# Performance work log

Hardware: AMD Instinct MI355X
Metric: run time of the kernel (lower is better)

The kernel has to match this reference:

```python
import jax, jax.numpy as jnp
import numpy as np


def setup_inputs() -> dict:
    key = jax.random.key(0)
    k1, k2 = jax.random.split(key)
    x1 = jax.random.normal(k1, (8192, 256), dtype=jnp.float32)
    x2 = jax.random.normal(k2, (8192, 256), dtype=jnp.float32)
    return {"x1": x1, "x2": x2}


def reference(x1, x2):
    # Euclidean distance matrix, equivalent to torch.cdist(x1, x2, p=2.0).
    # GEMM-based expansion: ||a-b||^2 = ||a||^2 + ||b||^2 - 2 a.b
    sq1 = jnp.sum(x1 * x1, axis=-1, keepdims=True)          # [N, 1]
    sq2 = jnp.sum(x2 * x2, axis=-1, keepdims=True)          # [M, 1]
    cross = jnp.einsum('nd,md->nm', x1, x2)                 # [N, M]
    d2 = sq1 + sq2.T - 2.0 * cross
    d2 = jnp.maximum(d2, 0.0)  # guard tiny negatives from cancellation
    return jnp.sqrt(d2)
```

## Files before the change

### kernel.cpp

```cpp
#include <hip/hip_runtime.h>


typedef __bf16 v8bf __attribute__((ext_vector_type(8)));
typedef float v4f __attribute__((ext_vector_type(4)));

#define NROWS 8192
#define KDIM  256
#define TILE  128
#define BK    64

typedef const __attribute__((address_space(1))) ushort* gas_ushort_p;
typedef __attribute__((address_space(3))) ushort* las_ushort_p;

__device__ __forceinline__ void async_load16(const ushort* g, ushort* l) {
    __builtin_amdgcn_global_load_lds((gas_ushort_p)g, (las_ushort_p)l, 16, 0, 0);
}

__device__ __forceinline__ ushort f2bf_rne(float f) {
    union { float f; unsigned u; } a; a.f = f;
    unsigned u = a.u + 0x7fffu + ((a.u >> 16) & 1u);
    return (ushort)(u >> 16);
}

__global__ __launch_bounds__(256) void cvt_norm_kernel(
    const float* __restrict__ x, ushort* __restrict__ xb, float* __restrict__ sq) {
    const int wave = threadIdx.x >> 6;
    const int lane = threadIdx.x & 63;
    const int row  = blockIdx.x * 4 + wave;
    const float4 v = ((const float4*)(x + (size_t)row * KDIM))[lane];
    float s = v.x * v.x + v.y * v.y + v.z * v.z + v.w * v.w;
#pragma unroll
    for (int off = 32; off; off >>= 1) s += __shfl_down(s, off);
    if (lane == 0) sq[row] = s;
    ushort4 o;
    o.x = f2bf_rne(v.x); o.y = f2bf_rne(v.y);
    o.z = f2bf_rne(v.z); o.w = f2bf_rne(v.w);
    ((ushort4*)(xb + (size_t)row * KDIM))[lane] = o;
}

__global__ __launch_bounds__(256) void cdist_mfma_kernel(
    const ushort* __restrict__ A,
    const ushort* __restrict__ B,
    const float* __restrict__ sq1,
    const float* __restrict__ sq2,
    float* __restrict__ out) {
    __shared__ ushort As[TILE * BK];
    __shared__ ushort Bs[TILE * BK];

    const int bm = blockIdx.x, bn = blockIdx.y;
    const int tid  = threadIdx.x;
    const int wave = tid >> 6;
    const int lane = tid & 63;
    const int wr = wave >> 1;
    const int wc = wave & 1;

    const int lrow = lane >> 3;
    const int lk   = (lane & 7) * 8;

    v4f acc[4][4];
#pragma unroll
    for (int i = 0; i < 4; ++i)
#pragma unroll
        for (int j = 0; j < 4; ++j) acc[i][j] = (v4f){0.f, 0.f, 0.f, 0.f};

    const int half = lane >> 4;
    const int mrow = lane & 15;

    for (int kt = 0; kt < KDIM; kt += BK) {
        __syncthreads();
#pragma unroll
        for (int c = 0; c < 4; ++c) {
            const int rbase = wave * 32 + c * 8;
            const ushort* ga =
                A + (size_t)(bm * TILE + rbase + lrow) * KDIM + kt + lk;
            const ushort* gb =
                B + (size_t)(bn * TILE + rbase + lrow) * KDIM + kt + lk;
            async_load16(ga, &As[rbase * BK]);
            async_load16(gb, &Bs[rbase * BK]);
        }
        __syncthreads();
#pragma unroll
        for (int kk = 0; kk < BK; kk += 32) {
            v8bf a[4], b[4];
#pragma unroll
            for (int i = 0; i < 4; ++i) {
                a[i] = *(const v8bf*)&As[(wr * 64 + i * 16 + mrow) * BK + kk + half * 8];
                b[i] = *(const v8bf*)&Bs[(wc * 64 + i * 16 + mrow) * BK + kk + half * 8];
            }
#pragma unroll
            for (int i = 0; i < 4; ++i)
#pragma unroll
                for (int j = 0; j < 4; ++j)
                    acc[i][j] = __builtin_amdgcn_mfma_f32_16x16x32_bf16(
                        a[i], b[j], acc[i][j], 0, 0, 0);
        }
    }

    const int m0 = bm * TILE + wr * 64;
    const int n0 = bn * TILE + wc * 64;
#pragma unroll
    for (int j = 0; j < 4; ++j) {
        const int col = n0 + j * 16 + mrow;
        const float s2 = sq2[col];
#pragma unroll
        for (int i = 0; i < 4; ++i) {
#pragma unroll
            for (int r = 0; r < 4; ++r) {
                const int row = m0 + i * 16 + half * 4 + r;
                const float d2 = sq1[row] + s2 - 2.0f * acc[i][j][r];
                out[(size_t)row * NROWS + col] = sqrtf(fmaxf(d2, 0.0f));
            }
        }
    }
}

extern "C" void kernel_launch(void* const* d_in, const int* in_sizes, int n_in,
                              void* d_out, int out_size, void* d_ws, size_t ws_size,
                              hipStream_t stream) {
    const float* x1 = (const float*)d_in[0];
    const float* x2 = (const float*)d_in[1];
    float* out = (float*)d_out;

    ushort* Ab = (ushort*)d_ws;
    ushort* Bb = Ab + (size_t)NROWS * KDIM;
    float* sq1 = (float*)(Bb + (size_t)NROWS * KDIM);
    float* sq2 = sq1 + NROWS;

    cvt_norm_kernel<<<NROWS / 4, 256, 0, stream>>>(x1, Ab, sq1);
    cvt_norm_kernel<<<NROWS / 4, 256, 0, stream>>>(x2, Bb, sq2);

    dim3 grid(NROWS / TILE, NROWS / TILE);
    cdist_mfma_kernel<<<grid, 256, 0, stream>>>(Ab, Bb, sq1, sq2, out);
}
```

Before: 357.4 us.

## Load MFMA operands directly from global memory, drop LDS staging, use nontemporal stores

Removes the LDS tiles and the async global-to-LDS copies with their two barriers per K-step. Each wave now loads its bf16 fragments straight from global memory (relying on L1/L2 for reuse) and runs the full K loop unrolled. The epilogue is reordered so sq2 values are hoisted, and the output is written with nontemporal stores. This trades explicit LDS sharing between waves for duplicate global/L2 traffic.

```diff
diff --git a/kernel.cpp b/kernel.cpp
--- a/kernel.cpp
+++ b/kernel.cpp
@@ -7,14 +7,6 @@
 #define NROWS 8192
 #define KDIM  256
 #define TILE  128
-#define BK    64
-
-typedef const __attribute__((address_space(1))) ushort* gas_ushort_p;
-typedef __attribute__((address_space(3))) ushort* las_ushort_p;
-
-__device__ __forceinline__ void async_load16(const ushort* g, ushort* l) {
-    __builtin_amdgcn_global_load_lds((gas_ushort_p)g, (las_ushort_p)l, 16, 0, 0);
-}
 
 __device__ __forceinline__ ushort f2bf_rne(float f) {
     union { float f; unsigned u; } a; a.f = f;
@@ -44,9 +36,6 @@
     const float* __restrict__ sq1,
     const float* __restrict__ sq2,
     float* __restrict__ out) {
-    __shared__ ushort As[TILE * BK];
-    __shared__ ushort Bs[TILE * BK];
-
     const int bm = blockIdx.x, bn = blockIdx.y;
     const int tid  = threadIdx.x;
     const int wave = tid >> 6;
@@ -54,8 +43,13 @@
     const int wr = wave >> 1;
     const int wc = wave & 1;
 
-    const int lrow = lane >> 3;
-    const int lk   = (lane & 7) * 8;
+    const int half = lane >> 4;
+    const int mrow = lane & 15;
+
+    const ushort* a_base =
+        A + (size_t)(bm * TILE + wr * 64 + mrow) * KDIM + half * 8;
+    const ushort* b_base =
+        B + (size_t)(bn * TILE + wc * 64 + mrow) * KDIM + half * 8;
 
     v4f acc[4][4];
 #pragma unroll
@@ -63,52 +57,40 @@
 #pragma unroll
         for (int j = 0; j < 4; ++j) acc[i][j] = (v4f){0.f, 0.f, 0.f, 0.f};
 
-    const int half = lane >> 4;
-    const int mrow = lane & 15;
-
-    for (int kt = 0; kt < KDIM; kt += BK) {
-        __syncthreads();
 #pragma unroll
-        for (int c = 0; c < 4; ++c) {
-            const int rbase = wave * 32 + c * 8;
-            const ushort* ga =
-                A + (size_t)(bm * TILE + rbase + lrow) * KDIM + kt + lk;
-            const ushort* gb =
-                B + (size_t)(bn * TILE + rbase + lrow) * KDIM + kt + lk;
-            async_load16(ga, &As[rbase * BK]);
-            async_load16(gb, &Bs[rbase * BK]);
-        }
-        __syncthreads();
+    for (int kt = 0; kt < KDIM; kt += 32) {
+        v8bf a[4], b[4];
 #pragma unroll
-        for (int kk = 0; kk < BK; kk += 32) {
-            v8bf a[4], b[4];
+        for (int i = 0; i < 4; ++i)
+            a[i] = *(const v8bf*)(a_base + (size_t)i * 16 * KDIM + kt);
 #pragma unroll
-            for (int i = 0; i < 4; ++i) {
-                a[i] = *(const v8bf*)&As[(wr * 64 + i * 16 + mrow) * BK + kk + half * 8];
-                b[i] = *(const v8bf*)&Bs[(wc * 64 + i * 16 + mrow) * BK + kk + half * 8];
-            }
+        for (int i = 0; i < 4; ++i)
+            b[i] = *(const v8bf*)(b_base + (size_t)i * 16 * KDIM + kt);
 #pragma unroll
-            for (int i = 0; i < 4; ++i)
+        for (int i = 0; i < 4; ++i)
 #pragma unroll
-                for (int j = 0; j < 4; ++j)
-                    acc[i][j] = __builtin_amdgcn_mfma_f32_16x16x32_bf16(
-                        a[i], b[j], acc[i][j], 0, 0, 0);
-        }
+            for (int j = 0; j < 4; ++j)
+                acc[i][j] = __builtin_amdgcn_mfma_f32_16x16x32_bf16(
+                    a[i], b[j], acc[i][j], 0, 0, 0);
     }
 
     const int m0 = bm * TILE + wr * 64;
     const int n0 = bn * TILE + wc * 64;
+    float s2[4];
 #pragma unroll
-    for (int j = 0; j < 4; ++j) {
-        const int col = n0 + j * 16 + mrow;
-        const float s2 = sq2[col];
+    for (int j = 0; j < 4; ++j) s2[j] = sq2[n0 + j * 16 + mrow];
 #pragma unroll
-        for (int i = 0; i < 4; ++i) {
+    for (int i = 0; i < 4; ++i) {
 #pragma unroll
-            for (int r = 0; r < 4; ++r) {
-                const int row = m0 + i * 16 + half * 4 + r;
-                const float d2 = sq1[row] + s2 - 2.0f * acc[i][j][r];
-                out[(size_t)row * NROWS + col] = sqrtf(fmaxf(d2, 0.0f));
+        for (int r = 0; r < 4; ++r) {
+            const int row = m0 + i * 16 + half * 4 + r;
+            const float s1 = sq1[row];
+            float* orow = out + (size_t)row * NROWS + n0 + mrow;
+#pragma unroll
+            for (int j = 0; j < 4; ++j) {
+                const float d2 = s1 + s2[j] - 2.0f * acc[i][j][r];
+                __builtin_nontemporal_store(sqrtf(fmaxf(d2, 0.0f)),
+                                            orow + j * 16);
             }
         }
     }
```

Result: no change. 363.7 us (+1.7%).
